# Kernel tuning notes

Measured on AMD Instinct MI355X. Metric: run time of the kernel, lower is better.

The kernel has to match this reference:

```python
import jax, jax.numpy as jnp
import numpy as np

D_MODEL = 512
N_STATE = 64
EMB_DIM = 512
LN_EPS = 1e-5


def setup_inputs() -> dict:
    key = jax.random.key(0)
    ks = jax.random.split(key, 12)
    B, L, d, N, e = 8, 2048, D_MODEL, N_STATE, EMB_DIM
    x = jax.random.normal(ks[0], (B, L, d), dtype=jnp.float32)
    emb = jax.random.normal(ks[1], (B, e), dtype=jnp.float32)
    # S4D kernel params
    A_real = -0.5 * jnp.ones((d, N), dtype=jnp.float32)
    A_imag = jnp.pi * jnp.broadcast_to(jnp.arange(N, dtype=jnp.float32)[None, :], (d, N))
    C = jax.random.normal(ks[2], (d, N, 2), dtype=jnp.float32) * 0.5
    dt_min, dt_max = 0.001, 0.1
    log_dt = jax.random.uniform(ks[3], (d,), dtype=jnp.float32) * (np.log(dt_max) - np.log(dt_min)) + np.log(dt_min)
    B_ssm = jnp.ones((d, N), dtype=jnp.float32)  # buffer, treated as constant
    # block params
    D_skip = jax.random.normal(ks[4], (d,), dtype=jnp.float32) * 0.01
    ln_gamma = jnp.ones((d,), dtype=jnp.float32)
    ln_beta = jnp.zeros((d,), dtype=jnp.float32)
    lim_out = 1.0 / np.sqrt(d)
    W_out = jax.random.uniform(ks[5], (2 * d, d), dtype=jnp.float32, minval=-lim_out, maxval=lim_out)
    b_out = jax.random.uniform(ks[6], (2 * d,), dtype=jnp.float32, minval=-lim_out, maxval=lim_out)
    lim_f = 1.0 / np.sqrt(e)
    W_film = jax.random.uniform(ks[7], (2 * d, e), dtype=jnp.float32, minval=-lim_f, maxval=lim_f)
    b_film = jax.random.uniform(ks[8], (2 * d,), dtype=jnp.float32, minval=-lim_f, maxval=lim_f)
    return dict(x=x, emb=emb, A_real=A_real, A_imag=A_imag, C=C, log_dt=log_dt,
                B_ssm=B_ssm, D_skip=D_skip, ln_gamma=ln_gamma, ln_beta=ln_beta,
                W_out=W_out, b_out=b_out, W_film=W_film, b_film=b_film)


def reference(x, emb, A_real, A_imag, C, log_dt, B_ssm, D_skip, ln_gamma, ln_beta,
              W_out, b_out, W_film, b_film):
    Bsz, L, d = x.shape
    residual = x
    # LayerNorm
    mu = jnp.mean(x, axis=-1, keepdims=True)
    var = jnp.mean((x - mu) ** 2, axis=-1, keepdims=True)
    xn = (x - mu) * jax.lax.rsqrt(var + LN_EPS) * ln_gamma + ln_beta
    # S4D kernel: K[d,l] = Re( sum_n (C*B)[d,n] * exp(dt*A)[d,n]**l ) * dt[d]
    dt = jnp.exp(log_dt)                                 # (d,)
    A = A_real + 1j * A_imag                             # (d,N)
    dtA = A * dt[:, None]                                # (d,N)
    Cc = (C[..., 0] + 1j * C[..., 1]) * B_ssm            # (d,N) complex
    l = jnp.arange(L, dtype=jnp.float32)
    powers = jnp.exp(dtA[:, :, None] * l)                # (d,N,L) complex, A_bar**l
    K = jnp.einsum('dn,dnl->dl', Cc, powers).real * dt[:, None]  # (d,L)
    # FFT convolution (circular over 2L -> linear)
    x_t = jnp.transpose(xn, (0, 2, 1))                   # (B,d,L)
    K_f = jnp.fft.rfft(K, n=2 * L)                       # (d,L+1)
    x_f = jnp.fft.rfft(x_t, n=2 * L)                     # (B,d,L+1)
    y = jnp.fft.irfft(K_f[None] * x_f, n=2 * L)[..., :L] # (B,d,L)
    y = y + x_t * D_skip[None, :, None]
    y = jnp.transpose(y, (0, 2, 1))                      # (B,L,d)
    # FiLM conditioning
    film = jax.nn.silu(emb) @ W_film.T + b_film          # (B,2d)
    scale, shift = jnp.split(film, 2, axis=-1)
    y = y * (1.0 + scale[:, None, :]) + shift[:, None, :]
    # out_proj: Linear(d,2d) + GLU
    proj = y @ W_out.T + b_out                           # (B,L,2d)
    a, g = jnp.split(proj, 2, axis=-1)
    y = a * jax.nn.sigmoid(g)
    return residual + y
```

## Files before the change

### kernel.cpp

```cpp
#include <hip/hip_runtime.h>
#include <math.h>

typedef __attribute__((ext_vector_type(8))) short bf8v;
typedef __attribute__((ext_vector_type(4))) float f4v;

union BF8 { bf8v v; unsigned short e[8]; };

__device__ __forceinline__ float bf2f(unsigned short u) {
  union { unsigned int i; float f; } c; c.i = ((unsigned int)u) << 16; return c.f;
}
__device__ __forceinline__ unsigned short f2bf(float f) {
  union { float f; unsigned int i; } c; c.f = f;
  return (unsigned short)((c.i + 0x7fffu + ((c.i >> 16) & 1u)) >> 16);
}
__device__ __forceinline__ void gld16(const unsigned short* g, unsigned short* l) {
  __builtin_amdgcn_global_load_lds(
      (const __attribute__((address_space(1))) unsigned int*)g,
      (__attribute__((address_space(3))) unsigned int*)l, 16, 0, 0);
}

__global__ __launch_bounds__(256) void prelude_kernel(
    const float* __restrict__ emb, const float* __restrict__ Wf,
    const float* __restrict__ bfm, float* __restrict__ film,
    const float* __restrict__ W, unsigned short* __restrict__ Wb,
    const float* __restrict__ A_real, const float* __restrict__ A_imag,
    const float* __restrict__ Cc, const float* __restrict__ log_dt,
    const float* __restrict__ B_ssm, const float* __restrict__ D_skip,
    unsigned short* __restrict__ Pre, unsigned short* __restrict__ Pim,
    unsigned short* __restrict__ Mre, unsigned short* __restrict__ Mim,
    unsigned short* __restrict__ Tt, float* __restrict__ W64r, float* __restrict__ W64i,
    const float* __restrict__ x, const float* __restrict__ gamma,
    const float* __restrict__ beta, unsigned short* __restrict__ xT) {
  __shared__ __align__(16) char sh[16 * 520 * 2];
  const int blk = blockIdx.x;
  const int tid = threadIdx.x;
  if (blk < 2048) {
    const int gw = blk * 4 + (tid >> 6);
    const int lane = tid & 63;
    const int b = gw >> 10, j = gw & 1023;
    const float4* ep = (const float4*)(emb + (size_t)b * 512) + lane * 2;
    const float4* wp = (const float4*)(Wf + (size_t)j * 512) + lane * 2;
    float acc = 0.f;
    #pragma unroll
    for (int i = 0; i < 2; i++) {
      const float4 e = ep[i], w = wp[i];
      acc += (e.x / (1.f + __expf(-e.x))) * w.x;
      acc += (e.y / (1.f + __expf(-e.y))) * w.y;
      acc += (e.z / (1.f + __expf(-e.z))) * w.z;
      acc += (e.w / (1.f + __expf(-e.w))) * w.w;
    }
    #pragma unroll
    for (int off = 32; off >= 1; off >>= 1) acc += __shfl_xor(acc, off);
    if (lane == 0) film[(size_t)b * 1024 + j] = acc + bfm[j];
  } else if (blk < 2560) {
    const int i = (blk - 2048) * 256 + tid;
    const float4 v = ((const float4*)W)[i];
    uint2 pk;
    pk.x = (unsigned)f2bf(v.x) | ((unsigned)f2bf(v.y) << 16);
    pk.y = (unsigned)f2bf(v.z) | ((unsigned)f2bf(v.w) << 16);
    ((uint2*)Wb)[i] = pk;
  } else if (blk < 3072) {
    float* Ktl = (float*)sh;
    const int d = blk - 2560;
    const float dt = __expf(log_dt[d]);
    const int wv = tid >> 6, n = tid & 63;
    {
      const int dn = d * 64 + n;
      const float ar = dt * A_real[dn], ai = dt * A_imag[dn];
      const float bs = B_ssm[dn] * dt;
      const float c0 = Cc[dn * 2] * bs, c1 = Cc[dn * 2 + 1] * bs;
      #pragma unroll
      for (int i = 0; i < 16; i++) {
        const float tau = (float)(wv * 16 + i);
        const float ex = __expf(ar * tau);
        float sn, cs; __sincosf(ai * tau, &sn, &cs);
        float r = ex * (c0 * cs - c1 * sn);
        #pragma unroll
        for (int off = 32; off >= 1; off >>= 1) r += __shfl_xor(r, off);
        if (n == 0) Ktl[wv * 16 + i] = (wv * 16 + i == 0) ? (r + D_skip[d]) : r;
      }
    }
    __syncthreads();
    for (int g = tid; g < 512; g += 256) {
      const int nn = g >> 3, s0 = (g & 7) * 8;
      const int dn = d * 64 + nn;
      const float ar = dt * A_real[dn], ai = dt * A_imag[dn];
      union { unsigned short s[8]; uint4 u; } pr, pi;
      #pragma unroll
      for (int j = 0; j < 8; j++) {
        const float k = (float)(63 - (s0 + j));
        const float ex = __expf(ar * k);
        float sn, cs; __sincosf(ai * k, &sn, &cs);
        pr.s[j] = f2bf(ex * cs); pi.s[j] = f2bf(ex * sn);
      }
      *(uint4*)(Pre + (size_t)d * 4096 + nn * 64 + s0) = pr.u;
      *(uint4*)(Pim + (size_t)d * 4096 + nn * 64 + s0) = pi.u;
    }
    for (int g = tid; g < 512; g += 256) {
      const int t = g >> 3, n0 = (g & 7) * 8;
      union { unsigned short s[8]; uint4 u; } mr, mi;
      #pragma unroll
      for (int j = 0; j < 8; j++) {
        const int dn = d * 64 + n0 + j;
        const float ar = dt * A_real[dn], ai = dt * A_imag[dn];
        const float bs = B_ssm[dn] * dt;
        const float c0 = Cc[dn * 2] * bs, c1 = Cc[dn * 2 + 1] * bs;
        const float k = (float)(t + 1);
        const float ex = __expf(ar * k);
        float sn, cs; __sincosf(ai * k, &sn, &cs);
        mr.s[j] = f2bf(ex * (c0 * cs - c1 * sn));
        mi.s[j] = f2bf(-ex * (c0 * sn + c1 * cs));
      }
      *(uint4*)(Mre + (size_t)d * 4096 + t * 64 + n0) = mr.u;
      *(uint4*)(Mim + (size_t)d * 4096 + t * 64 + n0) = mi.u;
    }
    for (int g = tid; g < 512; g += 256) {
      const int t = g >> 3, s0 = (g & 7) * 8;
      union { unsigned short s[8]; uint4 u; } tv;
      #pragma unroll
      for (int j = 0; j < 8; j++) {
        const int s = s0 + j;
        tv.s[j] = (s <= t) ? f2bf(Ktl[t - s]) : (unsigned short)0;
      }
      *(uint4*)(Tt + (size_t)d * 4096 + t * 64 + s0) = tv.u;
    }
    if (tid < 64) {
      const int dn = d * 64 + tid;
      const float ex = __expf(dt * A_real[dn] * 64.f);
      float sn, cs; __sincosf(dt * A_imag[dn] * 64.f, &sn, &cs);
      W64r[d * 64 + tid] = ex * cs;
      W64i[d * 64 + tid] = ex * sn;
    }
  } else {
    unsigned short* t = (unsigned short*)sh;
    const int r0 = (blk - 3072) * 16;
    const int wv = tid >> 6, lane = tid & 63;
    const float4* gp = (const float4*)gamma + lane * 2;
    const float4* bp = (const float4*)beta  + lane * 2;
    const float4 g0 = gp[0], g1 = gp[1], bb0 = bp[0], bb1 = bp[1];
    #pragma unroll
    for (int i = 0; i < 4; i++) {
      const int r = wv * 4 + i;
      const float4* xr = (const float4*)(x + (size_t)(r0 + r) * 512) + lane * 2;
      const float4 v0 = xr[0], v1 = xr[1];
      float s  = v0.x + v0.y + v0.z + v0.w + v1.x + v1.y + v1.z + v1.w;
      float sq = v0.x*v0.x + v0.y*v0.y + v0.z*v0.z + v0.w*v0.w
               + v1.x*v1.x + v1.y*v1.y + v1.z*v1.z + v1.w*v1.w;
      #pragma unroll
      for (int off = 32; off >= 1; off >>= 1) {
        s  += __shfl_xor(s, off);
        sq += __shfl_xor(sq, off);
      }
      const float mu   = s * (1.f / 512.f);
      const float var  = sq * (1.f / 512.f) - mu * mu;
      const float rstd = rsqrtf(var + 1e-5f);
      uint4 pk;
      pk.x = (unsigned)f2bf((v0.x - mu) * rstd * g0.x + bb0.x)
           | ((unsigned)f2bf((v0.y - mu) * rstd * g0.y + bb0.y) << 16);
      pk.y = (unsigned)f2bf((v0.z - mu) * rstd * g0.z + bb0.z)
           | ((unsigned)f2bf((v0.w - mu) * rstd * g0.w + bb0.w) << 16);
      pk.z = (unsigned)f2bf((v1.x - mu) * rstd * g1.x + bb1.x)
           | ((unsigned)f2bf((v1.y - mu) * rstd * g1.y + bb1.y) << 16);
      pk.w = (unsigned)f2bf((v1.z - mu) * rstd * g1.z + bb1.z)
           | ((unsigned)f2bf((v1.w - mu) * rstd * g1.w + bb1.w) << 16);
      *(uint4*)&t[r * 520 + lane * 8] = pk;
    }
    __syncthreads();
    const int p = tid;
    union { unsigned short s[8]; uint4 u; } a0, a1, b0, b1;
    #pragma unroll
    for (int r = 0; r < 8; r++) {
      const unsigned v = *(const unsigned*)&t[r * 520 + p * 2];
      a0.s[r] = (unsigned short)(v & 0xffffu);
      b0.s[r] = (unsigned short)(v >> 16);
    }
    #pragma unroll
    for (int r = 0; r < 8; r++) {
      const unsigned v = *(const unsigned*)&t[(r + 8) * 520 + p * 2];
      a1.s[r] = (unsigned short)(v & 0xffffu);
      b1.s[r] = (unsigned short)(v >> 16);
    }
    unsigned short* o0 = xT + (size_t)(2 * p) * 16384 + r0;
    *(uint4*)o0 = a0.u; *(uint4*)(o0 + 8) = a1.u;
    unsigned short* o1 = xT + (size_t)(2 * p + 1) * 16384 + r0;
    *(uint4*)o1 = b0.u; *(uint4*)(o1 + 8) = b1.u;
  }
}

__global__ __launch_bounds__(256) void tr_kernel(const unsigned short* __restrict__ in,
    unsigned short* __restrict__ out, int R, int C) {
  __shared__ __align__(16) unsigned short t[64 * 72];
  const int c0 = blockIdx.x * 64, r0 = blockIdx.y * 64;
  const int tid = threadIdx.x;
  #pragma unroll
  for (int i = 0; i < 2; i++) {
    const int idx = tid + i * 256;
    const int r = idx >> 3, q = idx & 7;
    const uint4 v = *(const uint4*)(in + (size_t)(r0 + r) * C + c0 + q * 8);
    *(uint4*)&t[r * 72 + ((q ^ (r >> 3)) * 8)] = v;
  }
  __syncthreads();
  #pragma unroll
  for (int i = 0; i < 2; i++) {
    const int idx = tid + i * 256;
    const int c = idx >> 3, g = idx & 7;
    union { unsigned short s[8]; uint4 u; } pk;
    #pragma unroll
    for (int j = 0; j < 8; j++)
      pk.s[j] = t[(g * 8 + j) * 72 + (((c >> 3) ^ g) * 8) + (c & 7)];
    *(uint4*)(out + (size_t)(c0 + c) * R + r0 + g * 8) = pk.u;
  }
}

__global__ __launch_bounds__(256, 2) void ssm_kernel(
    const unsigned short* __restrict__ xT,
    const unsigned short* __restrict__ Pre, const unsigned short* __restrict__ Pim,
    const unsigned short* __restrict__ Mre, const unsigned short* __restrict__ Mim,
    const unsigned short* __restrict__ Tt,
    const float* __restrict__ W64r, const float* __restrict__ W64i,
    const float* __restrict__ film, unsigned short* __restrict__ y2) {
  extern __shared__ char smem[];
  unsigned short* Pr = (unsigned short*)smem;
  unsigned short* Pi = Pr + 64 * 68;
  unsigned short* Mr = Pi + 64 * 68;
  unsigned short* Mi = Mr + 64 * 68;
  unsigned short* Tl = Mi + 64 * 68;
  unsigned int*   Eb = (unsigned int*)(Tl + 64 * 68);

  const int d = blockIdx.x;
  const int tid = threadIdx.x;
  const int wv = tid >> 6, lane = tid & 63;
  const int n15 = lane & 15, quad = lane >> 4;
  const int j0 = wv * 32;
  const size_t dtab = (size_t)d * 4096;

  {
    const unsigned short* gt[5] = {Pre + dtab, Pim + dtab, Mre + dtab, Mim + dtab, Tt + dtab};
    unsigned short* lt[5] = {Pr, Pi, Mr, Mi, Tl};
    #pragma unroll
    for (int i = 0; i < 10; i++) {
      const int idx = tid + i * 256;
      const int tb = idx >> 9, r = (idx >> 3) & 63, g = idx & 7;
      const uint4 v = *(const uint4*)(gt[tb] + r * 64 + g * 8);
      *(uint4*)&lt[tb][r * 68 + g * 8] = v;
    }
  }
  bf8v Xf[2][2][2];
  #pragma unroll
  for (int h = 0; h < 2; h++)
    #pragma unroll
    for (int ct = 0; ct < 2; ct++)
      #pragma unroll
      for (int kq = 0; kq < 2; kq++)
        Xf[h][ct][kq] = *(const bf8v*)(xT + (size_t)d * 16384 +
            (h * 128 + j0 + ct * 16 + n15) * 64 + kq * 32 + quad * 8);
  __syncthreads();

  #pragma unroll
  for (int h = 0; h < 2; h++) {
    const int jg0 = h * 128;
    {
      f4v Er[4][2], Ei[4][2];
      #pragma unroll
      for (int a = 0; a < 4; a++)
        #pragma unroll
        for (int b2 = 0; b2 < 2; b2++) { Er[a][b2] = (f4v){0,0,0,0}; Ei[a][b2] = (f4v){0,0,0,0}; }
      #pragma unroll
      for (int mt = 0; mt < 4; mt++)
        #pragma unroll
        for (int kq = 0; kq < 2; kq++) {
          const bf8v pr = *(const bf8v*)&Pr[(mt * 16 + n15) * 68 + kq * 32 + quad * 8];
          const bf8v pi = *(const bf8v*)&Pi[(mt * 16 + n15) * 68 + kq * 32 + quad * 8];
          #pragma unroll
          for (int ct = 0; ct < 2; ct++) {
            Er[mt][ct] = __builtin_amdgcn_mfma_f32_16x16x32_bf16(pr, Xf[h][ct][kq], Er[mt][ct], 0, 0, 0);
            Ei[mt][ct] = __builtin_amdgcn_mfma_f32_16x16x32_bf16(pi, Xf[h][ct][kq], Ei[mt][ct], 0, 0, 0);
          }
        }
      #pragma unroll
      for (int mt = 0; mt < 4; mt++)
        #pragma unroll
        for (int ct = 0; ct < 2; ct++)
          #pragma unroll
          for (int i = 0; i < 4; i++) {
            const int row = mt * 16 + quad * 4 + i;
            const int col = j0 + ct * 16 + n15;
            Eb[row * 131 + col] =
                (unsigned)f2bf(Er[mt][ct][i]) | ((unsigned)f2bf(Ei[mt][ct][i]) << 16);
          }
    }
    __syncthreads();

    {
      const int n = lane, bp = wv;
      const float wre = W64r[d * 64 + n], wim = W64i[d * 64 + n];
      unsigned int* row = &Eb[n * 131 + bp * 32];
      float str = 0.f, sti = 0.f;
      #pragma unroll
      for (int c = 0; c < 32; c++) {
        const unsigned u = row[c];
        row[c] = (unsigned)f2bf(str) | ((unsigned)f2bf(sti) << 16);
        const float er = bf2f((unsigned short)(u & 0xffffu));
        const float ei = bf2f((unsigned short)(u >> 16));
        const float nr = er + wre * str - wim * sti;
        const float ni = ei + wre * sti + wim * str;
        str = nr; sti = ni;
      }
    }
    __syncthreads();

    f4v Y[4][2];
    #pragma unroll
    for (int a = 0; a < 4; a++)
      #pragma unroll
      for (int b2 = 0; b2 < 2; b2++) Y[a][b2] = (f4v){0,0,0,0};

    #pragma unroll
    for (int mt = 0; mt < 4; mt++)
      #pragma unroll
      for (int kq = 0; kq < 2; kq++) {
        const bf8v tf = *(const bf8v*)&Tl[(mt * 16 + n15) * 68 + kq * 32 + quad * 8];
        #pragma unroll
        for (int ct = 0; ct < 2; ct++)
          Y[mt][ct] = __builtin_amdgcn_mfma_f32_16x16x32_bf16(tf, Xf[h][ct][kq], Y[mt][ct], 0, 0, 0);
      }

    #pragma unroll
    for (int kq = 0; kq < 2; kq++) {
      BF8 ir[2], ii[2];
      #pragma unroll
      for (int ct = 0; ct < 2; ct++)
        #pragma unroll
        for (int jj = 0; jj < 8; jj++) {
          const unsigned u = Eb[(kq * 32 + quad * 8 + jj) * 131 + (j0 + ct * 16 + n15)];
          ir[ct].e[jj] = (unsigned short)(u & 0xffffu);
          ii[ct].e[jj] = (unsigned short)(u >> 16);
        }
      #pragma unroll
      for (int mt = 0; mt < 4; mt++) {
        const bf8v mr = *(const bf8v*)&Mr[(mt * 16 + n15) * 68 + kq * 32 + quad * 8];
        const bf8v mi = *(const bf8v*)&Mi[(mt * 16 + n15) * 68 + kq * 32 + quad * 8];
        #pragma unroll
        for (int ct = 0; ct < 2; ct++) {
          Y[mt][ct] = __builtin_amdgcn_mfma_f32_16x16x32_bf16(mr, ir[ct].v, Y[mt][ct], 0, 0, 0);
          Y[mt][ct] = __builtin_amdgcn_mfma_f32_16x16x32_bf16(mi, ii[ct].v, Y[mt][ct], 0, 0, 0);
        }
      }
    }

    #pragma unroll
    for (int ct = 0; ct < 2; ct++) {
      const int jglob = jg0 + j0 + ct * 16 + n15;
      const int b = jglob >> 5;
      const float scl = 1.f + film[b * 1024 + d];
      const float shf = film[b * 1024 + 512 + d];
      #pragma unroll
      for (int mt = 0; mt < 4; mt++) {
        union { unsigned short s[4]; uint2 u; } pk;
        #pragma unroll
        for (int i = 0; i < 4; i++)
          pk.s[i] = f2bf(fmaf(Y[mt][ct][i], scl, shf));
        *(uint2*)(y2 + (size_t)d * 16384 + jglob * 64 + mt * 16 + quad * 4) = pk.u;
      }
    }
    if (h == 0) __syncthreads();
  }
}

__global__ __launch_bounds__(256) void gemm_kernel(
    const unsigned short* __restrict__ y2n, const unsigned short* __restrict__ Wb,
    const float* __restrict__ bo, const float* __restrict__ x,
    float* __restrict__ out) {
  __shared__ __align__(16) unsigned short Al[256 * 64];
  __shared__ __align__(16) unsigned short Bl[128 * 64];
  const int m0 = blockIdx.x * 256, cp0 = blockIdx.y * 64;
  const int tid = threadIdx.x;
  const int wv = tid >> 6, lane = tid & 63;
  const int n15 = lane & 15, quad = lane >> 4;
  const int lr = lane >> 3;
  const int lg = lane & 7;
  const int sg = (lg ^ lr) * 8;

  f4v acc[4][8];
  #pragma unroll
  for (int mt = 0; mt < 4; mt++)
    #pragma unroll
    for (int t4 = 0; t4 < 8; t4++) acc[mt][t4] = (f4v){0.f, 0.f, 0.f, 0.f};

  for (int kk = 0; kk < 8; kk++) {
    #pragma unroll
    for (int i = 0; i < 8; i++) {
      const int row = wv * 64 + i * 8 + lr;
      gld16(y2n + (size_t)(m0 + row) * 512 + kk * 64 + sg, Al + (wv * 64 + i * 8) * 64);
    }
    #pragma unroll
    for (int i = 0; i < 4; i++) {
      const int row = wv * 32 + i * 8 + lr;
      const int cg = (row < 64) ? (cp0 + row) : (512 + cp0 + row - 64);
      gld16(Wb + (size_t)cg * 512 + kk * 64 + sg, Bl + (wv * 32 + i * 8) * 64);
    }
    __syncthreads();
    #pragma unroll
    for (int kq = 0; kq < 2; kq++) {
      bf8v av[4], bv[8];
      #pragma unroll
      for (int mt = 0; mt < 4; mt++) {
        const int row = wv * 64 + mt * 16 + n15;
        av[mt] = *(const bf8v*)&Al[row * 64 + (((kq * 4 + quad) ^ (row & 7)) * 8)];
      }
      #pragma unroll
      for (int t4 = 0; t4 < 8; t4++) {
        const int row = t4 * 16 + n15;
        bv[t4] = *(const bf8v*)&Bl[row * 64 + (((kq * 4 + quad) ^ (row & 7)) * 8)];
      }
      #pragma unroll
      for (int mt = 0; mt < 4; mt++)
        #pragma unroll
        for (int t4 = 0; t4 < 8; t4++)
          acc[mt][t4] = __builtin_amdgcn_mfma_f32_16x16x32_bf16(av[mt], bv[t4], acc[mt][t4], 0, 0, 0);
    }
    __syncthreads();
  }
  #pragma unroll
  for (int mt = 0; mt < 4; mt++) {
    const int mrow = m0 + wv * 64 + mt * 16 + quad * 4;
    #pragma unroll
    for (int t4 = 0; t4 < 4; t4++) {
      const int c = cp0 + t4 * 16 + n15;
      const float ba = bo[c], bg = bo[512 + c];
      #pragma unroll
      for (int i = 0; i < 4; i++) {
        const size_t off = (size_t)(mrow + i) * 512 + c;
        const float av2 = acc[mt][t4][i] + ba;
        const float gv = acc[mt][t4 + 4][i] + bg;
        out[off] = x[off] + av2 * (1.f / (1.f + __expf(-gv)));
      }
    }
  }
}

extern "C" void kernel_launch(void* const* d_in, const int* in_sizes, int n_in,
                              void* d_out, int out_size, void* d_ws, size_t ws_size,
                              hipStream_t stream) {
  const float* x      = (const float*)d_in[0];
  const float* emb    = (const float*)d_in[1];
  const float* A_real = (const float*)d_in[2];
  const float* A_imag = (const float*)d_in[3];
  const float* C      = (const float*)d_in[4];
  const float* log_dt = (const float*)d_in[5];
  const float* B_ssm  = (const float*)d_in[6];
  const float* D_skip = (const float*)d_in[7];
  const float* gamma  = (const float*)d_in[8];
  const float* beta   = (const float*)d_in[9];
  const float* W_out  = (const float*)d_in[10];
  const float* b_out  = (const float*)d_in[11];
  const float* W_film = (const float*)d_in[12];
  const float* b_film = (const float*)d_in[13];
  float* out = (float*)d_out;

  char* ws = (char*)d_ws;
  size_t o = 0;
  float*          film = (float*)(ws + o);          o += 32768;
  unsigned short* xT   = (unsigned short*)(ws + o); o += 16777216;
  unsigned short* Wb   = (unsigned short*)(ws + o); o += 1048576;
  unsigned short* Pre  = (unsigned short*)(ws + o); o += 4194304;
  unsigned short* Pim  = (unsigned short*)(ws + o); o += 4194304;
  unsigned short* Mre  = (unsigned short*)(ws + o); o += 4194304;
  unsigned short* Mim  = (unsigned short*)(ws + o); o += 4194304;
  unsigned short* Tt   = (unsigned short*)(ws + o); o += 4194304;
  float*          W64r = (float*)(ws + o);          o += 131072;
  float*          W64i = (float*)(ws + o);          o += 131072;
  unsigned short* y2   = (unsigned short*)(ws + o); o += 16777216;
  unsigned short* y2n  = (unsigned short*)(ws + o); o += 16777216;

  prelude_kernel<<<dim3(4096), dim3(256), 0, stream>>>(
      emb, W_film, b_film, film, W_out, Wb,
      A_real, A_imag, C, log_dt, B_ssm, D_skip,
      Pre, Pim, Mre, Mim, Tt, W64r, W64i,
      x, gamma, beta, xT);
  ssm_kernel<<<dim3(512), dim3(256), 77056, stream>>>(xT, Pre, Pim, Mre, Mim, Tt,
                                                      W64r, W64i, film, y2);
  tr_kernel<<<dim3(256, 8), dim3(256), 0, stream>>>(y2, y2n, 512, 16384);
  gemm_kernel<<<dim3(64, 8), dim3(256), 0, stream>>>(y2n, Wb, b_out, x, out);
}
```

Baseline: 196.1 us.

## Fuse y2 transpose into GEMM A-tile loading and halve GEMM M-tile

Removes the separate transpose kernel and its 16MB intermediate buffer. The GEMM now reads the d-major y2 directly with vector loads, transposes it in registers and writes it into a swizzled LDS layout. The M tile is halved to 128 rows, which doubles the grid and allows three blocks per CU for occupancy. The cost is register-staged A loads in place of async global-to-LDS loads, plus extra LDS write work and bank-conflict risk.

```diff
diff --git a/kernel.cpp b/kernel.cpp
--- a/kernel.cpp
+++ b/kernel.cpp
@@ -5,6 +5,7 @@
 typedef __attribute__((ext_vector_type(4))) float f4v;
 
 union BF8 { bf8v v; unsigned short e[8]; };
+union U4 { uint4 u; unsigned short e[8]; };
 
 __device__ __forceinline__ float bf2f(unsigned short u) {
   union { unsigned int i; float f; } c; c.i = ((unsigned int)u) << 16; return c.f;
@@ -187,31 +188,6 @@
   }
 }
 
-__global__ __launch_bounds__(256) void tr_kernel(const unsigned short* __restrict__ in,
-    unsigned short* __restrict__ out, int R, int C) {
-  __shared__ __align__(16) unsigned short t[64 * 72];
-  const int c0 = blockIdx.x * 64, r0 = blockIdx.y * 64;
-  const int tid = threadIdx.x;
-  #pragma unroll
-  for (int i = 0; i < 2; i++) {
-    const int idx = tid + i * 256;
-    const int r = idx >> 3, q = idx & 7;
-    const uint4 v = *(const uint4*)(in + (size_t)(r0 + r) * C + c0 + q * 8);
-    *(uint4*)&t[r * 72 + ((q ^ (r >> 3)) * 8)] = v;
-  }
-  __syncthreads();
-  #pragma unroll
-  for (int i = 0; i < 2; i++) {
-    const int idx = tid + i * 256;
-    const int c = idx >> 3, g = idx & 7;
-    union { unsigned short s[8]; uint4 u; } pk;
-    #pragma unroll
-    for (int j = 0; j < 8; j++)
-      pk.s[j] = t[(g * 8 + j) * 72 + (((c >> 3) ^ g) * 8) + (c & 7)];
-    *(uint4*)(out + (size_t)(c0 + c) * R + r0 + g * 8) = pk.u;
-  }
-}
-
 __global__ __launch_bounds__(256, 2) void ssm_kernel(
     const unsigned short* __restrict__ xT,
     const unsigned short* __restrict__ Pre, const unsigned short* __restrict__ Pim,
@@ -367,46 +343,55 @@
   }
 }
 
-__global__ __launch_bounds__(256) void gemm_kernel(
-    const unsigned short* __restrict__ y2n, const unsigned short* __restrict__ Wb,
+__global__ __launch_bounds__(256, 3) void gemm_kernel(
+    const unsigned short* __restrict__ y2, const unsigned short* __restrict__ Wb,
     const float* __restrict__ bo, const float* __restrict__ x,
     float* __restrict__ out) {
-  __shared__ __align__(16) unsigned short Al[256 * 64];
+  __shared__ __align__(16) unsigned short Al[128 * 64];
   __shared__ __align__(16) unsigned short Bl[128 * 64];
-  const int m0 = blockIdx.x * 256, cp0 = blockIdx.y * 64;
+  const int m0 = blockIdx.x * 128, cp0 = blockIdx.y * 64;
   const int tid = threadIdx.x;
   const int wv = tid >> 6, lane = tid & 63;
   const int n15 = lane & 15, quad = lane >> 4;
   const int lr = lane >> 3;
   const int lg = lane & 7;
   const int sg = (lg ^ lr) * 8;
-
-  f4v acc[4][8];
+  const int mg = tid & 15;
+  const int kg = tid >> 4;
+
+  f4v acc[2][8];
   #pragma unroll
-  for (int mt = 0; mt < 4; mt++)
-    #pragma unroll
-    for (int t4 = 0; t4 < 8; t4++) acc[mt][t4] = (f4v){0.f, 0.f, 0.f, 0.f};
+  for (int mi = 0; mi < 2; mi++)
+    #pragma unroll
+    for (int t4 = 0; t4 < 8; t4++) acc[mi][t4] = (f4v){0.f, 0.f, 0.f, 0.f};
 
   for (int kk = 0; kk < 8; kk++) {
-    #pragma unroll
-    for (int i = 0; i < 8; i++) {
-      const int row = wv * 64 + i * 8 + lr;
-      gld16(y2n + (size_t)(m0 + row) * 512 + kk * 64 + sg, Al + (wv * 64 + i * 8) * 64);
-    }
+    U4 q[4];
+    #pragma unroll
+    for (int r = 0; r < 4; r++)
+      q[r].u = *(const uint4*)(y2 + (size_t)(kk * 64 + kg * 4 + r) * 16384 + m0 + mg * 8);
     #pragma unroll
     for (int i = 0; i < 4; i++) {
       const int row = wv * 32 + i * 8 + lr;
       const int cg = (row < 64) ? (cp0 + row) : (512 + cp0 + row - 64);
       gld16(Wb + (size_t)cg * 512 + kk * 64 + sg, Bl + (wv * 32 + i * 8) * 64);
     }
+    #pragma unroll
+    for (int i = 0; i < 8; i++) {
+      const int m = mg * 8 + i;
+      union { unsigned short e[4]; uint2 u; } o;
+      o.e[0] = q[0].e[i]; o.e[1] = q[1].e[i]; o.e[2] = q[2].e[i]; o.e[3] = q[3].e[i];
+      *(uint2*)&Al[m * 64 + (((kg >> 1) ^ i ^ (mg & 7)) & 7) * 8 + (kg & 1) * 4] = o.u;
+    }
     __syncthreads();
     #pragma unroll
     for (int kq = 0; kq < 2; kq++) {
-      bf8v av[4], bv[8];
-      #pragma unroll
-      for (int mt = 0; mt < 4; mt++) {
-        const int row = wv * 64 + mt * 16 + n15;
-        av[mt] = *(const bf8v*)&Al[row * 64 + (((kq * 4 + quad) ^ (row & 7)) * 8)];
+      bf8v av[2], bv[8];
+      #pragma unroll
+      for (int mt = 0; mt < 2; mt++) {
+        const int row = wv * 32 + mt * 16 + n15;
+        const int g = kq * 4 + quad;
+        av[mt] = *(const bf8v*)&Al[row * 64 + (((g ^ (row & 7) ^ ((row >> 3) & 7)) & 7) * 8)];
       }
       #pragma unroll
       for (int t4 = 0; t4 < 8; t4++) {
@@ -414,7 +399,7 @@
         bv[t4] = *(const bf8v*)&Bl[row * 64 + (((kq * 4 + quad) ^ (row & 7)) * 8)];
       }
       #pragma unroll
-      for (int mt = 0; mt < 4; mt++)
+      for (int mt = 0; mt < 2; mt++)
         #pragma unroll
         for (int t4 = 0; t4 < 8; t4++)
           acc[mt][t4] = __builtin_amdgcn_mfma_f32_16x16x32_bf16(av[mt], bv[t4], acc[mt][t4], 0, 0, 0);
@@ -422,8 +407,8 @@
     __syncthreads();
   }
   #pragma unroll
-  for (int mt = 0; mt < 4; mt++) {
-    const int mrow = m0 + wv * 64 + mt * 16 + quad * 4;
+  for (int mt = 0; mt < 2; mt++) {
+    const int mrow = m0 + wv * 32 + mt * 16 + quad * 4;
     #pragma unroll
     for (int t4 = 0; t4 < 4; t4++) {
       const int c = cp0 + t4 * 16 + n15;
@@ -471,7 +456,6 @@
   float*          W64r = (float*)(ws + o);          o += 131072;
   float*          W64i = (float*)(ws + o);          o += 131072;
   unsigned short* y2   = (unsigned short*)(ws + o); o += 16777216;
-  unsigned short* y2n  = (unsigned short*)(ws + o); o += 16777216;
 
   prelude_kernel<<<dim3(4096), dim3(256), 0, stream>>>(
       emb, W_film, b_film, film, W_out, Wb,
@@ -480,6 +464,5 @@
       x, gamma, beta, xT);
   ssm_kernel<<<dim3(512), dim3(256), 77056, stream>>>(xT, Pre, Pim, Mre, Mim, Tt,
                                                       W64r, W64i, film, y2);
-  tr_kernel<<<dim3(256, 8), dim3(256), 0, stream>>>(y2, y2n, 512, 16384);
-  gemm_kernel<<<dim3(64, 8), dim3(256), 0, stream>>>(y2n, Wb, b_out, x, out);
-}
+  gemm_kernel<<<dim3(128, 8), dim3(256), 0, stream>>>(y2, Wb, b_out, x, out);
+}
```

Result: faster. 184.5 us (-5.9%).
